# Kernel optimization log

Hardware: AMD Instinct MI355X
Metric: run time of the kernel (lower is better)

The kernel has to match this reference:

```python
import jax, jax.numpy as jnp
import numpy as np

B, T, C, H = 4096, 128, 128, 64  # T must equal BLOCK_SIZE=128, C=EMBEDDING_DIM=128


def setup_inputs() -> dict:
    key = jax.random.key(0)
    k1, k2, k3, k4, k5, k6 = jax.random.split(key, 6)
    source_embedding = jax.random.normal(k1, (B, T, C), dtype=jnp.float32)
    target_embedding = jax.random.normal(k2, (B, T, C), dtype=jnp.float32)
    # realistic padding: positions < length are valid; guarantees col 0 valid (no NaN rows)
    lengths = jax.random.randint(k3, (B,), 1, T + 1)
    pad_mask = jnp.arange(T)[None, :] < lengths[:, None]  # (B, T) bool
    Wq = jax.random.normal(k4, (C, H), dtype=jnp.float32) * 0.02
    Wk = jax.random.normal(k5, (C, H), dtype=jnp.float32) * 0.02
    Wv = jax.random.normal(k6, (C, H), dtype=jnp.float32) * 0.02
    return {"source_embedding": source_embedding, "target_embedding": target_embedding,
            "pad_mask": pad_mask, "Wq": Wq, "Wk": Wk, "Wv": Wv}


def reference(source_embedding, target_embedding, pad_mask, Wq, Wk, Wv):
    # q from target, k/v from source (cross-attention capable), bias-free projections
    q = target_embedding @ Wq   # (B, T, H)
    k = source_embedding @ Wk   # (B, T, H)
    v = source_embedding @ Wv   # (B, T, H)
    scale = k.shape[-1] ** -0.5
    wei = jnp.einsum('btd,bsd->bts', q, k) * scale  # (B, T, T)
    causal = jnp.tril(jnp.ones((T, T), dtype=bool))  # needs_future_mask=True
    mask = pad_mask[:, None, :] & causal[None, :, :]  # fuse pad + future masks
    wei = jnp.where(mask, wei, -jnp.inf)
    wei = jax.nn.softmax(wei, axis=-1)
    # dropout disabled (eval mode) for deterministic reference
    out = wei @ v  # (B, T, H)
    return out
```

## Files before the change

kernel.cpp:

```cpp
#include <hip/hip_runtime.h>
#include <stdint.h>


typedef uint32_t u32x2 __attribute__((ext_vector_type(2)));
typedef uint32_t u32x4 __attribute__((ext_vector_type(4)));
typedef float    f32x4 __attribute__((ext_vector_type(4)));
typedef __bf16   bf16x8 __attribute__((ext_vector_type(8)));

static __device__ __forceinline__ uint32_t pack2(float a, float b) {
  uint32_t ua = __builtin_bit_cast(uint32_t, a);
  uint32_t ub = __builtin_bit_cast(uint32_t, b);
  ua += 0x7FFFu + ((ua >> 16) & 1u);
  ub += 0x7FFFu + ((ub >> 16) & 1u);
  return (ua >> 16) | (ub & 0xFFFF0000u);
}
static __device__ __forceinline__ uint32_t cvt2(float a, float b) {
  uint16_t lo = __builtin_bit_cast(uint16_t, (__bf16)a);
  uint16_t hi = __builtin_bit_cast(uint16_t, (__bf16)b);
  return (uint32_t)lo | ((uint32_t)hi << 16);
}
static __device__ __forceinline__ f32x4 mfma16(u32x4 a, u32x4 b, f32x4 c) {
  return __builtin_amdgcn_mfma_f32_16x16x32_bf16(
      __builtin_bit_cast(bf16x8, a), __builtin_bit_cast(bf16x8, b), c, 0, 0, 0);
}

__global__ void prep_w(const float* __restrict__ Wq, const float* __restrict__ Wk,
                       const float* __restrict__ Wv, const void* __restrict__ mask,
                       uint32_t* __restrict__ ws) {
  const int blk = blockIdx.x;
  const int l = threadIdx.x;
  if (blk < 48) {
    const int m  = blk >> 4;
    const int ct = (blk >> 2) & 3;
    const int ks = blk & 3;
    const float* W = (m == 0) ? Wq : ((m == 1) ? Wk : Wv);
    const int h  = ct * 16 + (l & 15);
    const int c0 = ks * 32 + (l >> 4) * 8;
    u32x4 v;
#pragma unroll
    for (int p = 0; p < 4; ++p)
      v[p] = pack2(W[(c0 + 2 * p) * 64 + h], W[(c0 + 2 * p + 1) * 64 + h]);
    ((u32x4*)ws)[blk * 64 + l] = v;
  } else {
    const uint32_t* mw = (const uint32_t*)mask;
    int fl = 0;
    for (int i = l * 16; i < l * 16 + 16; ++i) {
      uint32_t x = mw[i];
      if (x == 0x3F800000u) fl = 2;
      else if (x > 1u && fl != 2) fl = 1;
    }
#pragma unroll
    for (int off = 32; off > 0; off >>= 1) {
      int o = __shfl_down(fl, off);
      fl = (o > fl) ? o : fl;
    }
    if (l == 0) ws[12288] = (uint32_t)fl;
  }
}

__global__ __launch_bounds__(512, 3) void attn_fused(
    const float* __restrict__ src, const float* __restrict__ tgt,
    const void* __restrict__ mask, const uint32_t* __restrict__ ws,
    float* __restrict__ out) {
  __shared__ __align__(16) uint8_t lds[49664];
  uint8_t* const EMB = lds;
  uint8_t* const Kb  = lds + 16384;
  uint8_t* const Vb  = lds + 32768;
  float*  const BIAS = (float*)(lds + 49152);

  const int b   = blockIdx.x;
  const int tid = (int)threadIdx.x;
  const int l   = tid & 63;
  const int w   = tid >> 6;
  const int l15 = l & 15;
  const int g4  = l >> 4;
  const int ct  = w & 3;
  const int sg  = (w >> 2) * 2;
  const int tq  = 16 * w + l15;

  const u32x4* wsv = (const u32x4*)ws;
  const int mflag = (int)ws[12288];
  const float* const srcb = src + (size_t)b * 16384;
  const float* const tgtb = tgt + (size_t)b * 16384;

  f32x4 qv[8];
  {
    const float* pq = tgtb + tq * 128 + g4 * 8;
#pragma unroll
    for (int ks = 0; ks < 4; ++ks) {
      qv[2 * ks]     = *(const f32x4*)(pq + ks * 32);
      qv[2 * ks + 1] = *(const f32x4*)(pq + ks * 32 + 4);
    }
  }
  f32x4 pf[4];
  auto stage_load = [&](const float* gbase) {
#pragma unroll
    for (int p = 0; p < 4; ++p)
      pf[p] = *(const f32x4*)(gbase + tid * 4 + p * 2048);
  };
  stage_load(srcb);
  float biasv = 0.0f;
  if (tid < 128) {
    bool valid;
    if (mflag == 1)      valid = ((const uint8_t*)mask)[b * 128 + tid] != 0;
    else if (mflag == 0) valid = ((const int*)mask)[b * 128 + tid] != 0;
    else                 valid = ((const float*)mask)[b * 128 + tid] != 0.0f;
    biasv = valid ? 0.0f : -1e30f;
  }

  uint32_t qp[8];
  {
    f32x4 c0 = {0,0,0,0}, c1 = {0,0,0,0}, c2 = {0,0,0,0}, c3 = {0,0,0,0};
#pragma unroll
    for (int ks = 0; ks < 4; ++ks) {
      u32x4 e = { cvt2(qv[2*ks][0], qv[2*ks][1]), cvt2(qv[2*ks][2], qv[2*ks][3]),
                  cvt2(qv[2*ks+1][0], qv[2*ks+1][1]), cvt2(qv[2*ks+1][2], qv[2*ks+1][3]) };
      c0 = mfma16(wsv[(0  + ks) * 64 + l], e, c0);
      c1 = mfma16(wsv[(4  + ks) * 64 + l], e, c1);
      c2 = mfma16(wsv[(8  + ks) * 64 + l], e, c2);
      c3 = mfma16(wsv[(12 + ks) * 64 + l], e, c3);
    }
    qp[0] = cvt2(c0[0], c0[1]); qp[1] = cvt2(c0[2], c0[3]);
    qp[2] = cvt2(c1[0], c1[1]); qp[3] = cvt2(c1[2], c1[3]);
    qp[4] = cvt2(c2[0], c2[1]); qp[5] = cvt2(c2[2], c2[3]);
    qp[6] = cvt2(c3[0], c3[1]); qp[7] = cvt2(c3[2], c3[3]);
  }

  auto stage_write = [&]() {
#pragma unroll
    for (int p = 0; p < 4; ++p) {
      const int c   = tid + p * 512;
      const int row = c >> 5;
      const int cc  = c & 31;
      u32x2 d = { cvt2(pf[p][0], pf[p][1]), cvt2(pf[p][2], pf[p][3]) };
      *(u32x2*)(EMB + (row << 8) + ((((cc >> 1) ^ (row & 7))) << 4) + ((cc & 1) << 3)) = d;
    }
  };
  u32x4 wk[4], wv[4];
#pragma unroll
  for (int ks = 0; ks < 4; ++ks) {
    wk[ks] = wsv[((4 + ct) * 4 + ks) * 64 + l];
    wv[ks] = wsv[((8 + ct) * 4 + ks) * 64 + l];
  }
  auto projKV = [&](int half) {
#pragma unroll
    for (int i = 0; i < 2; ++i) {
      const int st  = sg + i;
      const int row = st * 16 + l15;
      f32x4 cK = {0, 0, 0, 0}, cV = {0, 0, 0, 0};
#pragma unroll
      for (int ks = 0; ks < 4; ++ks) {
        u32x4 e = *(const u32x4*)(EMB + (row << 8) + ((((ks * 4 + g4) ^ (row & 7))) << 4));
        cK = mfma16(wk[ks], e, cK);
        cV = mfma16(e, wv[ks], cV);
      }
      const int s  = half * 64 + st * 16 + l15;
      const int h0 = ct * 16 + g4 * 4;
      u32x2 dk = { cvt2(cK[0], cK[1]), cvt2(cK[2], cK[3]) };
      *(u32x2*)(Kb + (s << 7) + ((((h0 >> 3) ^ (s & 7))) << 4) + ((h0 & 7) << 1)) = dk;
      const int s0 = half * 64 + st * 16 + g4 * 4;
      const int h  = ct * 16 + l15;
      u32x2 dv = { cvt2(cV[0], cV[1]), cvt2(cV[2], cV[3]) };
      *(u32x2*)(Vb + (h << 8) + ((((s0 >> 3) ^ (h & 7))) << 4) + ((s0 & 7) << 1)) = dv;
    }
  };

  stage_write();
  if (tid < 128) BIAS[tid] = biasv;
  __syncthreads();
  stage_load(srcb + 8192);
  projKV(0);
  __syncthreads();
  stage_write();
  __syncthreads();
  projKV(1);
  __syncthreads();

  const int hi2 = g4 >> 1;
  const int sA  = ((g4 & 1) * 2) * 16 + l15;
  const int sB  = sA + 16;

  u32x4 qB[2];
#pragma unroll
  for (int ks = 0; ks < 2; ++ks) {
    uint32_t a0 = (uint32_t)__shfl((int)qp[4 * ks + 0], sA);
    uint32_t a1 = (uint32_t)__shfl((int)qp[4 * ks + 1], sA);
    uint32_t a2 = (uint32_t)__shfl((int)qp[4 * ks + 2], sA);
    uint32_t a3 = (uint32_t)__shfl((int)qp[4 * ks + 3], sA);
    uint32_t b0 = (uint32_t)__shfl((int)qp[4 * ks + 0], sB);
    uint32_t b1 = (uint32_t)__shfl((int)qp[4 * ks + 1], sB);
    uint32_t b2 = (uint32_t)__shfl((int)qp[4 * ks + 2], sB);
    uint32_t b3 = (uint32_t)__shfl((int)qp[4 * ks + 3], sB);
    qB[ks][0] = hi2 ? a2 : a0;
    qB[ks][1] = hi2 ? a3 : a1;
    qB[ks][2] = hi2 ? b2 : b0;
    qB[ks][3] = hi2 ? b3 : b1;
  }

  f32x4 sacc[8];
#pragma unroll
  for (int mt = 0; mt < 8; ++mt) sacc[mt] = {0, 0, 0, 0};
  __builtin_amdgcn_s_setprio(1);
#pragma unroll
  for (int mt = 0; mt < 8; ++mt) {
    const int srow = mt * 16 + l15;
    u32x4 k0 = *(const u32x4*)(Kb + (srow << 7) + (((g4 ^ (srow & 7))) << 4));
    u32x4 k1 = *(const u32x4*)(Kb + (srow << 7) + ((((4 + g4) ^ (srow & 7))) << 4));
    sacc[mt] = mfma16(k0, qB[0], sacc[mt]);
    sacc[mt] = mfma16(k1, qB[1], sacc[mt]);
  }
  __builtin_amdgcn_s_setprio(0);

  float m = -3.0e38f;
#pragma unroll
  for (int mt = 0; mt < 8; ++mt) {
    f32x4 b4 = *(const f32x4*)(BIAS + mt * 16 + g4 * 4);
#pragma unroll
    for (int r = 0; r < 4; ++r) {
      float v = sacc[mt][r] * 0.125f + b4[r];
      sacc[mt][r] = v;
      m = fmaxf(m, v);
    }
  }
  m = fmaxf(m, __shfl_xor(m, 16));
  m = fmaxf(m, __shfl_xor(m, 32));
  float sum = 0.0f;
#pragma unroll
  for (int mt = 0; mt < 8; ++mt) {
#pragma unroll
    for (int r = 0; r < 4; ++r) {
      const int s = mt * 16 + g4 * 4 + r;
      float p = __expf(sacc[mt][r] - m);
      p = (s <= tq) ? p : 0.0f;
      sacc[mt][r] = p;
      sum += p;
    }
  }
  sum += __shfl_xor(sum, 16);
  sum += __shfl_xor(sum, 32);
  const float inv = 1.0f / sum;

  uint32_t sp[16];
#pragma unroll
  for (int mt = 0; mt < 8; ++mt) {
    sp[2 * mt]     = cvt2(sacc[mt][0], sacc[mt][1]);
    sp[2 * mt + 1] = cvt2(sacc[mt][2], sacc[mt][3]);
  }

  f32x4 oacc[4];
#pragma unroll
  for (int vt = 0; vt < 4; ++vt) oacc[vt] = {0, 0, 0, 0};
  __builtin_amdgcn_s_setprio(1);
#pragma unroll
  for (int ks = 0; ks < 4; ++ks) {
    uint32_t a0 = (uint32_t)__shfl((int)sp[4 * ks + 0], sA);
    uint32_t a1 = (uint32_t)__shfl((int)sp[4 * ks + 1], sA);
    uint32_t a2 = (uint32_t)__shfl((int)sp[4 * ks + 2], sA);
    uint32_t a3 = (uint32_t)__shfl((int)sp[4 * ks + 3], sA);
    uint32_t b0 = (uint32_t)__shfl((int)sp[4 * ks + 0], sB);
    uint32_t b1 = (uint32_t)__shfl((int)sp[4 * ks + 1], sB);
    uint32_t b2 = (uint32_t)__shfl((int)sp[4 * ks + 2], sB);
    uint32_t b3 = (uint32_t)__shfl((int)sp[4 * ks + 3], sB);
    u32x4 pb;
    pb[0] = hi2 ? a2 : a0;
    pb[1] = hi2 ? a3 : a1;
    pb[2] = hi2 ? b2 : b0;
    pb[3] = hi2 ? b3 : b1;
#pragma unroll
    for (int vt = 0; vt < 4; ++vt) {
      const int vrow = vt * 16 + l15;
      u32x4 vf = *(const u32x4*)(Vb + (vrow << 8) + ((((ks * 4 + g4) ^ (vrow & 7))) << 4));
      oacc[vt] = mfma16(vf, pb, oacc[vt]);
    }
  }
  __builtin_amdgcn_s_setprio(0);

  float* const ob = out + (size_t)b * 8192 + (size_t)tq * 64;
#pragma unroll
  for (int vt = 0; vt < 4; ++vt) {
    f32x4 o = { oacc[vt][0] * inv, oacc[vt][1] * inv,
                oacc[vt][2] * inv, oacc[vt][3] * inv };
    *(f32x4*)(ob + vt * 16 + g4 * 4) = o;
  }
}

extern "C" void kernel_launch(void* const* d_in, const int* in_sizes, int n_in,
                              void* d_out, int out_size, void* d_ws, size_t ws_size,
                              hipStream_t stream) {
  const float* src = (const float*)d_in[0];
  const float* tgt = (const float*)d_in[1];
  const void*  msk = d_in[2];
  const float* Wq  = (const float*)d_in[3];
  const float* Wk  = (const float*)d_in[4];
  const float* Wv  = (const float*)d_in[5];
  uint32_t* ws = (uint32_t*)d_ws;
  float* out = (float*)d_out;
  const int B = in_sizes[0] / (128 * 128);

  hipLaunchKernelGGL(prep_w, dim3(49), dim3(64), 0, stream, Wq, Wk, Wv, msk, ws);
  hipLaunchKernelGGL(attn_fused, dim3(B), dim3(512), 0, stream,
                     src, tgt, msk, ws, out);
}
```

Baseline: 154.1 us.

## Stage whole source tile in LDS at once and pass P through LDS

Doubles the embedding staging buffer so all 128 source rows are converted and written to LDS in one pass. This cuts the two-phase load/project sequence down to one barrier before the K/V projection. The Q projection now sits after the K/V projection, and the P-to-B-operand transpose goes through a per-wave LDS scratch region reusing EMB instead of many cross-lane shuffles. The cost is more LDS per block (about 66KB), so occupancy drops from 3 to 2 blocks per CU and register pressure is higher from holding 8 prefetched vectors.

New measurement: 154.4 us. About the same (+0.2%).

```diff
diff --git a/kernel.cpp b/kernel.cpp
--- a/kernel.cpp
+++ b/kernel.cpp
@@ -58,15 +58,15 @@
   }
 }
 
-__global__ __launch_bounds__(512, 3) void attn_fused(
+__global__ __launch_bounds__(512, 2) void attn_fused(
     const float* __restrict__ src, const float* __restrict__ tgt,
     const void* __restrict__ mask, const uint32_t* __restrict__ ws,
     float* __restrict__ out) {
-  __shared__ __align__(16) uint8_t lds[49664];
+  __shared__ __align__(16) uint8_t lds[66048];
   uint8_t* const EMB = lds;
-  uint8_t* const Kb  = lds + 16384;
-  uint8_t* const Vb  = lds + 32768;
-  float*  const BIAS = (float*)(lds + 49152);
+  uint8_t* const Kb  = lds + 32768;
+  uint8_t* const Vb  = lds + 49152;
+  float*  const BIAS = (float*)(lds + 65536);
 
   const int b   = blockIdx.x;
   const int tid = (int)threadIdx.x;
@@ -92,13 +92,10 @@
       qv[2 * ks + 1] = *(const f32x4*)(pq + ks * 32 + 4);
     }
   }
-  f32x4 pf[4];
-  auto stage_load = [&](const float* gbase) {
-#pragma unroll
-    for (int p = 0; p < 4; ++p)
-      pf[p] = *(const f32x4*)(gbase + tid * 4 + p * 2048);
-  };
-  stage_load(srcb);
+  f32x4 pf[8];
+#pragma unroll
+  for (int p = 0; p < 8; ++p)
+    pf[p] = *(const f32x4*)(srcb + tid * 4 + p * 2048);
   float biasv = 0.0f;
   if (tid < 128) {
     bool valid;
@@ -108,6 +105,47 @@
     biasv = valid ? 0.0f : -1e30f;
   }
 
+#pragma unroll
+  for (int p = 0; p < 8; ++p) {
+    const int c   = tid + p * 512;
+    const int row = c >> 5;
+    const int cc  = c & 31;
+    u32x2 d = { cvt2(pf[p][0], pf[p][1]), cvt2(pf[p][2], pf[p][3]) };
+    *(u32x2*)(EMB + (row << 8) + ((((cc >> 1) ^ (row & 7))) << 4) + ((cc & 1) << 3)) = d;
+  }
+  if (tid < 128) BIAS[tid] = biasv;
+  __syncthreads();
+
+  u32x4 wk[4], wv[4];
+#pragma unroll
+  for (int ks = 0; ks < 4; ++ks) {
+    wk[ks] = wsv[((4 + ct) * 4 + ks) * 64 + l];
+    wv[ks] = wsv[((8 + ct) * 4 + ks) * 64 + l];
+  }
+#pragma unroll
+  for (int half = 0; half < 2; ++half) {
+#pragma unroll
+    for (int i = 0; i < 2; ++i) {
+      const int s16 = half * 64 + (sg + i) * 16;
+      const int row = s16 + l15;
+      f32x4 cK = {0, 0, 0, 0}, cV = {0, 0, 0, 0};
+#pragma unroll
+      for (int ks = 0; ks < 4; ++ks) {
+        u32x4 e = *(const u32x4*)(EMB + (row << 8) + ((((ks * 4 + g4) ^ (row & 7))) << 4));
+        cK = mfma16(wk[ks], e, cK);
+        cV = mfma16(e, wv[ks], cV);
+      }
+      const int s  = row;
+      const int h0 = ct * 16 + g4 * 4;
+      u32x2 dk = { cvt2(cK[0], cK[1]), cvt2(cK[2], cK[3]) };
+      *(u32x2*)(Kb + (s << 7) + ((((h0 >> 3) ^ (s & 7))) << 4) + ((h0 & 7) << 1)) = dk;
+      const int s0 = s16 + g4 * 4;
+      const int h  = ct * 16 + l15;
+      u32x2 dv = { cvt2(cV[0], cV[1]), cvt2(cV[2], cV[3]) };
+      *(u32x2*)(Vb + (h << 8) + ((((s0 >> 3) ^ (h & 7))) << 4) + ((s0 & 7) << 1)) = dv;
+    }
+  }
+
   uint32_t qp[8];
   {
     f32x4 c0 = {0,0,0,0}, c1 = {0,0,0,0}, c2 = {0,0,0,0}, c3 = {0,0,0,0};
@@ -126,60 +164,9 @@
     qp[6] = cvt2(c3[0], c3[1]); qp[7] = cvt2(c3[2], c3[3]);
   }
 
-  auto stage_write = [&]() {
-#pragma unroll
-    for (int p = 0; p < 4; ++p) {
-      const int c   = tid + p * 512;
-      const int row = c >> 5;
-      const int cc  = c & 31;
-      u32x2 d = { cvt2(pf[p][0], pf[p][1]), cvt2(pf[p][2], pf[p][3]) };
-      *(u32x2*)(EMB + (row << 8) + ((((cc >> 1) ^ (row & 7))) << 4) + ((cc & 1) << 3)) = d;
-    }
-  };
-  u32x4 wk[4], wv[4];
-#pragma unroll
-  for (int ks = 0; ks < 4; ++ks) {
-    wk[ks] = wsv[((4 + ct) * 4 + ks) * 64 + l];
-    wv[ks] = wsv[((8 + ct) * 4 + ks) * 64 + l];
-  }
-  auto projKV = [&](int half) {
-#pragma unroll
-    for (int i = 0; i < 2; ++i) {
-      const int st  = sg + i;
-      const int row = st * 16 + l15;
-      f32x4 cK = {0, 0, 0, 0}, cV = {0, 0, 0, 0};
-#pragma unroll
-      for (int ks = 0; ks < 4; ++ks) {
-        u32x4 e = *(const u32x4*)(EMB + (row << 8) + ((((ks * 4 + g4) ^ (row & 7))) << 4));
-        cK = mfma16(wk[ks], e, cK);
-        cV = mfma16(e, wv[ks], cV);
-      }
-      const int s  = half * 64 + st * 16 + l15;
-      const int h0 = ct * 16 + g4 * 4;
-      u32x2 dk = { cvt2(cK[0], cK[1]), cvt2(cK[2], cK[3]) };
-      *(u32x2*)(Kb + (s << 7) + ((((h0 >> 3) ^ (s & 7))) << 4) + ((h0 & 7) << 1)) = dk;
-      const int s0 = half * 64 + st * 16 + g4 * 4;
-      const int h  = ct * 16 + l15;
-      u32x2 dv = { cvt2(cV[0], cV[1]), cvt2(cV[2], cV[3]) };
-      *(u32x2*)(Vb + (h << 8) + ((((s0 >> 3) ^ (h & 7))) << 4) + ((s0 & 7) << 1)) = dv;
-    }
-  };
-
-  stage_write();
-  if (tid < 128) BIAS[tid] = biasv;
-  __syncthreads();
-  stage_load(srcb + 8192);
-  projKV(0);
-  __syncthreads();
-  stage_write();
-  __syncthreads();
-  projKV(1);
-  __syncthreads();
-
   const int hi2 = g4 >> 1;
   const int sA  = ((g4 & 1) * 2) * 16 + l15;
   const int sB  = sA + 16;
-
   u32x4 qB[2];
 #pragma unroll
   for (int ks = 0; ks < 2; ++ks) {
@@ -197,6 +184,8 @@
     qB[ks][3] = hi2 ? b3 : b1;
   }
 
+  __syncthreads();
+
   f32x4 sacc[8];
 #pragma unroll
   for (int mt = 0; mt < 8; ++mt) sacc[mt] = {0, 0, 0, 0};
@@ -240,11 +229,12 @@
   sum += __shfl_xor(sum, 32);
   const float inv = 1.0f / sum;
 
-  uint32_t sp[16];
-#pragma unroll
-  for (int mt = 0; mt < 8; ++mt) {
-    sp[2 * mt]     = cvt2(sacc[mt][0], sacc[mt][1]);
-    sp[2 * mt + 1] = cvt2(sacc[mt][2], sacc[mt][3]);
+  uint8_t* const Pr = EMB + (w << 12) + (l15 << 8);
+#pragma unroll
+  for (int mt = 0; mt < 8; ++mt) {
+    u32x2 d = { cvt2(sacc[mt][0], sacc[mt][1]), cvt2(sacc[mt][2], sacc[mt][3]) };
+    const int c = mt * 2 + (g4 >> 1);
+    *(u32x2*)(Pr + (((c ^ l15)) << 4) + ((g4 & 1) << 3)) = d;
   }
 
   f32x4 oacc[4];
@@ -253,19 +243,7 @@
   __builtin_amdgcn_s_setprio(1);
 #pragma unroll
   for (int ks = 0; ks < 4; ++ks) {
-    uint32_t a0 = (uint32_t)__shfl((int)sp[4 * ks + 0], sA);
-    uint32_t a1 = (uint32_t)__shfl((int)sp[4 * ks + 1], sA);
-    uint32_t a2 = (uint32_t)__shfl((int)sp[4 * ks + 2], sA);
-    uint32_t a3 = (uint32_t)__shfl((int)sp[4 * ks + 3], sA);
-    uint32_t b0 = (uint32_t)__shfl((int)sp[4 * ks + 0], sB);
-    uint32_t b1 = (uint32_t)__shfl((int)sp[4 * ks + 1], sB);
-    uint32_t b2 = (uint32_t)__shfl((int)sp[4 * ks + 2], sB);
-    uint32_t b3 = (uint32_t)__shfl((int)sp[4 * ks + 3], sB);
-    u32x4 pb;
-    pb[0] = hi2 ? a2 : a0;
-    pb[1] = hi2 ? a3 : a1;
-    pb[2] = hi2 ? b2 : b0;
-    pb[3] = hi2 ? b3 : b1;
+    u32x4 pb = *(const u32x4*)(Pr + ((((ks * 4 + g4) ^ l15)) << 4));
 #pragma unroll
     for (int vt = 0; vt < 4; ++vt) {
       const int vrow = vt * 16 + l15;
```
